# Performance work log

Measured on AMD Instinct MI355X. Metric: run time of the kernel, lower is better.

Reference implementation:

```python
import jax, jax.numpy as jnp
import numpy as np

NUM_USERS = 100000
NUM_ITEMS = 100000
EMBED_F = 64
BATCH = 8192
MAX_HIST = 200
MU = 3.5


def setup_inputs() -> dict:
    key = jax.random.key(0)
    ks = jax.random.split(key, 9)
    inv_f = 1.0 / EMBED_F
    return {
        "user": jax.random.randint(ks[0], (BATCH,), 0, NUM_USERS),
        "item": jax.random.randint(ks[1], (BATCH,), 0, NUM_ITEMS),
        "implicit": jax.random.randint(ks[2], (BATCH, MAX_HIST), 0, NUM_ITEMS),
        "hist_len": jax.random.randint(ks[3], (BATCH,), 0, MAX_HIST),
        "P": jax.random.normal(ks[4], (NUM_USERS, EMBED_F), dtype=jnp.float32) * inv_f,
        "Q": jax.random.normal(ks[5], (NUM_ITEMS, EMBED_F), dtype=jnp.float32) * inv_f,
        "Y": jax.random.normal(ks[6], (NUM_ITEMS, EMBED_F), dtype=jnp.float32) * inv_f,
        "bu": jax.random.normal(ks[7], (NUM_USERS,), dtype=jnp.float32),
        "bi": jax.random.normal(ks[8], (NUM_ITEMS,), dtype=jnp.float32),
    }


def reference(user, item, implicit, hist_len, P, Q, Y, bu, bi):
    # lengths clamped to >=1 (original assumes every user has implicit feedback)
    lengths = jnp.maximum(hist_len, 1)                      # [B]
    mask = (jnp.arange(MAX_HIST)[None, :] < lengths[:, None]).astype(P.dtype)  # [B,H]

    # baseline estimate: mu + b_u + b_i
    bui = MU + bu[user] + bi[item]                          # [B]

    P_u = P[user]                                           # [B,F]
    Q_i = Q[item]                                           # [B,F]

    # ragged embedding-bag sum over implicit items (masked gather+sum)
    Y_g = Y[implicit]                                       # [B,H,F]
    y_sum = jnp.einsum("bhf,bh->bf", Y_g, mask)             # [B,F]
    norm = lengths.astype(P.dtype) ** -0.5                  # [B]

    rui = bui + jnp.sum(P_u * (Q_i + norm[:, None] * y_sum), axis=1)
    return rui
```

## Files before the change

kernel.cpp:

```cpp
#include <hip/hip_runtime.h>

#define BATCH_SZ 8192
#define MAX_HIST 200
#define EMBED_F 64

__device__ __forceinline__ float4 f4add(float4 a, float4 b) {
    return make_float4(a.x + b.x, a.y + b.y, a.z + b.z, a.w + b.w);
}

__global__ __launch_bounds__(128) void svdpp_kernel(
    const int*   __restrict__ user,
    const int*   __restrict__ item,
    const int*   __restrict__ implicit,
    const int*   __restrict__ hist_len,
    const float* __restrict__ P,
    const float* __restrict__ Q,
    const float* __restrict__ Y,
    const float* __restrict__ bu,
    const float* __restrict__ bi,
    float*       __restrict__ out)
{
    __shared__ int    lds_idx[MAX_HIST];
    __shared__ float4 lds_part[16];

    const int b    = (int)blockIdx.x;
    const int w    = (int)(threadIdx.x >> 6);
    const int lane = (int)(threadIdx.x & 63);
    const int g = lane >> 4;
    const int s = lane & 15;

    const int L = max(hist_len[b], 1);

    int u = 0, it = 0;
    float4 pu = make_float4(0.f, 0.f, 0.f, 0.f);
    float4 qi = make_float4(0.f, 0.f, 0.f, 0.f);
    float bub = 0.f, bib = 0.f;
    if (w == 0) {
        u  = user[b];
        it = item[b];
        pu = reinterpret_cast<const float4*>(P)[(size_t)u  * 16 + s];
        qi = reinterpret_cast<const float4*>(Q)[(size_t)it * 16 + s];
        bub = bu[u];
        bib = bi[it];
    }

    const int* idx_row = implicit + (size_t)b * MAX_HIST;
    if (threadIdx.x < MAX_HIST / 4) {
        int4 v = *reinterpret_cast<const int4*>(idx_row + threadIdx.x * 4);
        *reinterpret_cast<int4*>(&lds_idx[threadIdx.x * 4]) = v;
    }
    __syncthreads();

    const float4* __restrict__ Y4 = reinterpret_cast<const float4*>(Y);

    const int full   = L >> 2;
    const int npacks = (L + 3) >> 2;

    float4 acc = make_float4(0.f, 0.f, 0.f, 0.f);
    int p = w;

    for (; p + 14 < full; p += 16) {
        float4 y[8];
        #pragma unroll
        for (int j = 0; j < 8; ++j) {
            const int i = lds_idx[4 * (p + 2 * j) + g];
            y[j] = Y4[(size_t)i * 16 + s];
        }
        acc = f4add(acc, f4add(f4add(f4add(y[0], y[1]), f4add(y[2], y[3])),
                               f4add(f4add(y[4], y[5]), f4add(y[6], y[7]))));
    }
    for (; p + 6 < full; p += 8) {
        float4 y[4];
        #pragma unroll
        for (int j = 0; j < 4; ++j) {
            const int i = lds_idx[4 * (p + 2 * j) + g];
            y[j] = Y4[(size_t)i * 16 + s];
        }
        acc = f4add(acc, f4add(f4add(y[0], y[1]), f4add(y[2], y[3])));
    }
    for (; p < npacks; p += 2) {
        const int i = lds_idx[4 * p + g];
        const float4 y = Y4[(size_t)i * 16 + s];
        if (4 * p + g < L) acc = f4add(acc, y);
    }

    #pragma unroll
    for (int off = 16; off < 64; off <<= 1) {
        acc.x += __shfl_xor(acc.x, off, 64);
        acc.y += __shfl_xor(acc.y, off, 64);
        acc.z += __shfl_xor(acc.z, off, 64);
        acc.w += __shfl_xor(acc.w, off, 64);
    }

    if (w == 1 && lane < 16) lds_part[s] = acc;
    __syncthreads();
    if (w == 0) {
        const float4 o = lds_part[s];
        acc = f4add(acc, o);

        const float norm = 1.0f / sqrtf((float)L);
        float v = pu.x * (qi.x + norm * acc.x)
                + pu.y * (qi.y + norm * acc.y)
                + pu.z * (qi.z + norm * acc.z)
                + pu.w * (qi.w + norm * acc.w);

        #pragma unroll
        for (int off = 1; off < 16; off <<= 1)
            v += __shfl_xor(v, off, 64);

        if (lane == 0)
            out[b] = 3.5f + bub + bib + v;
    }
}

extern "C" void kernel_launch(void* const* d_in, const int* in_sizes, int n_in,
                              void* d_out, int out_size, void* d_ws, size_t ws_size,
                              hipStream_t stream) {
    const int*   user     = (const int*)  d_in[0];
    const int*   item     = (const int*)  d_in[1];
    const int*   implicit = (const int*)  d_in[2];
    const int*   hist_len = (const int*)  d_in[3];
    const float* P        = (const float*)d_in[4];
    const float* Q        = (const float*)d_in[5];
    const float* Y        = (const float*)d_in[6];
    const float* bu       = (const float*)d_in[7];
    const float* bi       = (const float*)d_in[8];
    float* out = (float*)d_out;

    svdpp_kernel<<<BATCH_SZ, 128, 0, stream>>>(
        user, item, implicit, hist_len, P, Q, Y, bu, bi, out);
}
```

Baseline: 136.0 us.

## Map one wavefront per batch row, packing four rows per block

```diff
diff --git a/kernel.cpp b/kernel.cpp
--- a/kernel.cpp
+++ b/kernel.cpp
@@ -3,12 +3,13 @@
 #define BATCH_SZ 8192
 #define MAX_HIST 200
 #define EMBED_F 64
+#define WPB 4
 
 __device__ __forceinline__ float4 f4add(float4 a, float4 b) {
     return make_float4(a.x + b.x, a.y + b.y, a.z + b.z, a.w + b.w);
 }
 
-__global__ __launch_bounds__(128) void svdpp_kernel(
+__global__ __launch_bounds__(256) void svdpp_kernel(
     const int*   __restrict__ user,
     const int*   __restrict__ item,
     const int*   __restrict__ implicit,
@@ -20,66 +21,61 @@
     const float* __restrict__ bi,
     float*       __restrict__ out)
 {
-    __shared__ int    lds_idx[MAX_HIST];
-    __shared__ float4 lds_part[16];
+    __shared__ int lds_idx[WPB][MAX_HIST];
 
-    const int b    = (int)blockIdx.x;
     const int w    = (int)(threadIdx.x >> 6);
     const int lane = (int)(threadIdx.x & 63);
+    const int b    = (int)blockIdx.x * WPB + w;
     const int g = lane >> 4;
     const int s = lane & 15;
 
     const int L = max(hist_len[b], 1);
 
-    int u = 0, it = 0;
-    float4 pu = make_float4(0.f, 0.f, 0.f, 0.f);
-    float4 qi = make_float4(0.f, 0.f, 0.f, 0.f);
-    float bub = 0.f, bib = 0.f;
-    if (w == 0) {
-        u  = user[b];
-        it = item[b];
-        pu = reinterpret_cast<const float4*>(P)[(size_t)u  * 16 + s];
-        qi = reinterpret_cast<const float4*>(Q)[(size_t)it * 16 + s];
-        bub = bu[u];
-        bib = bi[it];
+    const int* idx_row = implicit + (size_t)b * MAX_HIST;
+    if (lane < MAX_HIST / 4) {
+        int4 v = *reinterpret_cast<const int4*>(idx_row + lane * 4);
+        *reinterpret_cast<int4*>(&lds_idx[w][lane * 4]) = v;
     }
 
-    const int* idx_row = implicit + (size_t)b * MAX_HIST;
-    if (threadIdx.x < MAX_HIST / 4) {
-        int4 v = *reinterpret_cast<const int4*>(idx_row + threadIdx.x * 4);
-        *reinterpret_cast<int4*>(&lds_idx[threadIdx.x * 4]) = v;
-    }
+    const int u  = user[b];
+    const int it = item[b];
+    const float4 pu = reinterpret_cast<const float4*>(P)[(size_t)u  * 16 + s];
+    const float4 qi = reinterpret_cast<const float4*>(Q)[(size_t)it * 16 + s];
+    const float bub = bu[u];
+    const float bib = bi[it];
+
     __syncthreads();
 
     const float4* __restrict__ Y4 = reinterpret_cast<const float4*>(Y);
+    const int* my_idx = lds_idx[w];
 
     const int full   = L >> 2;
     const int npacks = (L + 3) >> 2;
 
     float4 acc = make_float4(0.f, 0.f, 0.f, 0.f);
-    int p = w;
+    int p = 0;
 
-    for (; p + 14 < full; p += 16) {
+    for (; p + 7 < full; p += 8) {
         float4 y[8];
         #pragma unroll
         for (int j = 0; j < 8; ++j) {
-            const int i = lds_idx[4 * (p + 2 * j) + g];
+            const int i = my_idx[4 * (p + j) + g];
             y[j] = Y4[(size_t)i * 16 + s];
         }
         acc = f4add(acc, f4add(f4add(f4add(y[0], y[1]), f4add(y[2], y[3])),
                                f4add(f4add(y[4], y[5]), f4add(y[6], y[7]))));
     }
-    for (; p + 6 < full; p += 8) {
+    for (; p + 3 < full; p += 4) {
         float4 y[4];
         #pragma unroll
         for (int j = 0; j < 4; ++j) {
-            const int i = lds_idx[4 * (p + 2 * j) + g];
+            const int i = my_idx[4 * (p + j) + g];
             y[j] = Y4[(size_t)i * 16 + s];
         }
         acc = f4add(acc, f4add(f4add(y[0], y[1]), f4add(y[2], y[3])));
     }
-    for (; p < npacks; p += 2) {
-        const int i = lds_idx[4 * p + g];
+    for (; p < npacks; ++p) {
+        const int i = my_idx[4 * p + g];
         const float4 y = Y4[(size_t)i * 16 + s];
         if (4 * p + g < L) acc = f4add(acc, y);
     }
@@ -92,25 +88,18 @@
         acc.w += __shfl_xor(acc.w, off, 64);
     }
 
-    if (w == 1 && lane < 16) lds_part[s] = acc;
-    __syncthreads();
-    if (w == 0) {
-        const float4 o = lds_part[s];
-        acc = f4add(acc, o);
+    const float norm = 1.0f / sqrtf((float)L);
+    float v = pu.x * (qi.x + norm * acc.x)
+            + pu.y * (qi.y + norm * acc.y)
+            + pu.z * (qi.z + norm * acc.z)
+            + pu.w * (qi.w + norm * acc.w);
 
-        const float norm = 1.0f / sqrtf((float)L);
-        float v = pu.x * (qi.x + norm * acc.x)
-                + pu.y * (qi.y + norm * acc.y)
-                + pu.z * (qi.z + norm * acc.z)
-                + pu.w * (qi.w + norm * acc.w);
+    #pragma unroll
+    for (int off = 1; off < 16; off <<= 1)
+        v += __shfl_xor(v, off, 64);
 
-        #pragma unroll
-        for (int off = 1; off < 16; off <<= 1)
-            v += __shfl_xor(v, off, 64);
-
-        if (lane == 0)
-            out[b] = 3.5f + bub + bib + v;
-    }
+    if (lane == 0)
+        out[b] = 3.5f + bub + bib + v;
 }
 
 extern "C" void kernel_launch(void* const* d_in, const int* in_sizes, int n_in,
@@ -127,6 +116,6 @@
     const float* bi       = (const float*)d_in[8];
     float* out = (float*)d_out;
 
-    svdpp_kernel<<<BATCH_SZ, 128, 0, stream>>>(
+    svdpp_kernel<<<BATCH_SZ / WPB, 256, 0, stream>>>(
         user, item, implicit, hist_len, P, Q, Y, bu, bi, out);
 }
```

Result: no change. 136.6 us (+0.5%).
